# Kernel optimization log

Hardware: AMD Instinct MI355X
Metric: run time of the kernel (lower is better)

The kernel has to match this reference:

```python
import jax, jax.numpy as jnp
import numpy as np

D_IN = 1024
D_OUT = 1024


def setup_inputs() -> dict:
    key = jax.random.key(0)
    kx, kq, kk, kv = jax.random.split(key, 4)
    B, T = 8, 2048
    x = jax.random.normal(kx, (B, T, D_IN), dtype=jnp.float32)
    # torch Linear weight is (d_out, d_in); we store transposed (d_in, d_out)
    s = 1.0 / np.sqrt(D_IN)
    Wq = jax.random.uniform(kq, (D_IN, D_OUT), jnp.float32, -s, s)
    Wk = jax.random.uniform(kk, (D_IN, D_OUT), jnp.float32, -s, s)
    Wv = jax.random.uniform(kv, (D_IN, D_OUT), jnp.float32, -s, s)
    return {"x": x, "Wq": Wq, "Wk": Wk, "Wv": Wv}


def reference(x, Wq, Wk, Wv):
    # x: (B, T, d_in)
    T = x.shape[1]
    d_out = Wq.shape[1]
    q = jnp.einsum('btd,de->bte', x, Wq)  # (B,T,d_out)
    k = jnp.einsum('btd,de->bte', x, Wk)
    v = jnp.einsum('btd,de->bte', x, Wv)
    scores = jnp.einsum('bqe,bke->bqk', q, k)  # (B,T,T)
    causal = jnp.tril(jnp.ones((T, T), dtype=bool))  # True = keep
    scores = jnp.where(causal[None], scores, -jnp.inf)
    weights = jax.nn.softmax(scores / jnp.sqrt(jnp.asarray(d_out, x.dtype)), axis=-1)
    # dropout p=0.0 -> identity
    return jnp.einsum('bqk,bke->bqe', weights, v)  # (B,T,d_out)
```

## Files before the change

### kernel.cpp

```cpp
#include <hip/hip_runtime.h>

using u16 = unsigned short;
typedef __bf16 bf16x8 __attribute__((ext_vector_type(8)));
typedef unsigned short u16x8 __attribute__((ext_vector_type(8)));
typedef float floatx4 __attribute__((ext_vector_type(4)));

__device__ __forceinline__ u16 f2bf(float f) {
  union { float f; unsigned u; } c; c.f = f;
  unsigned u = c.u;
  u += 0x7fffu + ((u >> 16) & 1u);
  return (u16)(u >> 16);
}
__device__ __forceinline__ float bf2f(u16 h) {
  union { unsigned u; float f; } c; c.u = ((unsigned)h) << 16; return c.f;
}

__device__ __forceinline__ void st_out(float* p, float v) { *p = v; }
__device__ __forceinline__ void st_out(u16* p, float v) { *p = f2bf(v); }

__device__ __forceinline__ void load16(const u16* g, u16* l) {
  __builtin_amdgcn_global_load_lds(
      (const __attribute__((address_space(1))) void*)g,
      (__attribute__((address_space(3))) void*)l, 16, 0, 0);
}

#define TILE 128
#define BK 64

template<typename OutT>
__device__ __forceinline__ void gemm_core(
    const u16* __restrict__ A, int lda, long sA,
    const u16* __restrict__ Bt, int ldb, long sB,
    OutT* __restrict__ C, int ldc, long sC,
    int kmax, int bx, int by, int bz, int tid)
{
  __shared__ u16 As[TILE * BK];
  __shared__ u16 Bs[TILE * BK];

  const u16* Ab = A + bz * sA + (long)by * TILE * lda;
  const u16* Bb = Bt + bz * sB + (long)bx * TILE * ldb;

  int lane = tid & 63;
  int wm = ((tid >> 7) & 1) * 64;
  int wn = ((tid >> 6) & 1) * 64;

  floatx4 acc[4][4] = {};
  int arow = wm + (lane & 15);
  int brow = wn + (lane & 15);
  int q = lane >> 4;

  for (int k0 = 0; k0 < kmax; k0 += BK) {
    __syncthreads();
#pragma unroll
    for (int h = 0; h < 4; h++) {
      int cc = tid + h * 256;
      int row = cc >> 3, gm = (cc & 7) ^ (row & 7);
      load16(Ab + (long)row * lda + k0 + gm * 8, &As[cc * 8]);
    }
#pragma unroll
    for (int h = 0; h < 4; h++) {
      int cc = tid + h * 256;
      int row = cc >> 3, gm = (cc & 7) ^ (row & 7);
      load16(Bb + (long)row * ldb + k0 + gm * 8, &Bs[cc * 8]);
    }
    __builtin_amdgcn_s_waitcnt(0);
    __syncthreads();

#pragma unroll
    for (int kp = 0; kp < 2; kp++) {
      bf16x8 a[4], b[4];
#pragma unroll
      for (int i = 0; i < 4; i++) {
        int r = arow + i * 16;
        a[i] = *(const bf16x8*)&As[(r * 8 + ((kp * 4 + q) ^ (r & 7))) * 8];
      }
#pragma unroll
      for (int j = 0; j < 4; j++) {
        int r = brow + j * 16;
        b[j] = *(const bf16x8*)&Bs[(r * 8 + ((kp * 4 + q) ^ (r & 7))) * 8];
      }
#pragma unroll
      for (int i = 0; i < 4; i++)
#pragma unroll
        for (int j = 0; j < 4; j++)
          acc[i][j] = __builtin_amdgcn_mfma_f32_16x16x32_bf16(a[i], b[j], acc[i][j], 0, 0, 0);
    }
  }

  OutT* Cb = C + bz * sC;
  int colbase = bx * TILE + wn + (lane & 15);
  int rowbase = by * TILE + wm + ((lane >> 4) << 2);
#pragma unroll
  for (int i = 0; i < 4; i++)
#pragma unroll
    for (int j = 0; j < 4; j++) {
      int col = colbase + j * 16;
#pragma unroll
      for (int r = 0; r < 4; r++)
        st_out(&Cb[(long)(rowbase + i * 16 + r) * ldc + col], acc[i][j][r]);
    }
}

template<typename OutT>
__global__ __launch_bounds__(256, 2)
void gemm_rect(const u16* __restrict__ A, int lda, long sA,
               const u16* __restrict__ Bt, int ldb, long sB,
               OutT* __restrict__ C, int ldc, long sC, int K,
               int l2gx, int nO8s)
{
  int L = blockIdx.x;
  int t = ((L & 7) << nO8s) | (L >> 3);
  int bx = t & ((1 << l2gx) - 1), by = t >> l2gx;
  gemm_core<OutT>(A, lda, sA, Bt, ldb, sB, C, ldc, sC, K, bx, by, blockIdx.y, threadIdx.x);
}

__global__ __launch_bounds__(256, 2)
void gemm_proj(const u16* __restrict__ xb, const u16* __restrict__ NT,
               const u16* __restrict__ WvT, u16* __restrict__ Yb,
               u16* __restrict__ VT)
{
  int L = blockIdx.x;
  bool h = (L >= 1024);
  int LL = h ? L - 1024 : L;
  int t = ((LL & 7) << 7) | (LL >> 3);
  int bx = h ? (t & 127) : (t & 7);
  int by = h ? (t >> 7) : (t >> 3);
  gemm_core<u16>(h ? WvT : xb, 1024, 0L,
                 h ? xb : NT, 1024, 0L,
                 h ? VT : Yb, h ? 16384 : 1024, 0L,
                 1024, bx, by, 0, threadIdx.x);
}

__global__ __launch_bounds__(256, 2)
void gemm_tri(const u16* __restrict__ A, int lda, long sA,
              const u16* __restrict__ Bt, int ldb, long sB,
              u16* __restrict__ C, int ldc, long sC, int K)
{
  int tp = blockIdx.x;
  int t = (tp & 7) * 17 + (tp >> 3);
  int r = (int)((sqrtf(8.f * t + 1.f) - 1.f) * 0.5f);
  while ((r + 1) * (r + 2) / 2 <= t) ++r;
  while (r * (r + 1) / 2 > t) --r;
  int c = t - r * (r + 1) / 2;
  gemm_core<u16>(A, lda, sA, Bt, ldb, sB, C, ldc, sC, K, c, r, blockIdx.y, threadIdx.x);
}

__global__ __launch_bounds__(256, 2)
void gemm_opv(const u16* __restrict__ P, int lda, long sA,
              const u16* __restrict__ VT, int ldb, long sB,
              float* __restrict__ C, int ldc, long sC)
{
  int L = blockIdx.x;
  int j = L & 7, s = L >> 3;
  int by = (s < 8) ? 15 - j : j;
  int bx = s & 7;
  gemm_core<float>(P, lda, sA, VT, ldb, sB, C, ldc, sC,
                   (by + 1) * TILE, bx, by, blockIdx.y, threadIdx.x);
}

__global__ __launch_bounds__(256)
void cvt_x(const float4* __restrict__ x, u16* __restrict__ o, int n4, float scale)
{
  int i = blockIdx.x * 256 + threadIdx.x;
  if (i >= n4) return;
  float4 v = x[i];
  ushort4 r;
  r.x = f2bf(v.x * scale); r.y = f2bf(v.y * scale);
  r.z = f2bf(v.z * scale); r.w = f2bf(v.w * scale);
  *(ushort4*)(o + (long)i * 4) = r;
}

__global__ __launch_bounds__(256)
void cvt_w(const float* __restrict__ W, u16* __restrict__ O)
{
  const int D = 1024;
  __shared__ float t[64][65];
  int tid = threadIdx.x;
  int c = tid & 63, r = tid >> 6;
  int e0 = blockIdx.x * 64, d0 = blockIdx.y * 64;
  for (int rr = r; rr < 64; rr += 4)
    t[rr][c] = W[(long)(d0 + rr) * D + e0 + c];
  __syncthreads();
  for (int rr = r; rr < 64; rr += 4)
    O[(long)(e0 + rr) * D + d0 + c] = f2bf(t[c][rr]);
}

__global__ __launch_bounds__(256)
void softmax_bf16(u16* __restrict__ S)
{
  const int T = 2048;
  int row = blockIdx.x & (T - 1);
  u16* Prow = S + (long)blockIdx.x * T;
  int n = row + 1;
  int tid = threadIdx.x, lane = tid & 63, wid = tid >> 6;
  int i0 = tid * 8;

  u16x8 pv = *(const u16x8*)(Prow + i0);
  float v[8];
  float lmax = -3.0e38f;
#pragma unroll
  for (int j = 0; j < 8; j++) {
    v[j] = (i0 + j < n) ? bf2f(pv[j]) : -3.0e38f;
    lmax = fmaxf(lmax, v[j]);
  }
  __shared__ float red[8];
#pragma unroll
  for (int o = 32; o > 0; o >>= 1) lmax = fmaxf(lmax, __shfl_down(lmax, o, 64));
  if (lane == 0) red[wid] = lmax;
  __syncthreads();
  float m = fmaxf(fmaxf(red[0], red[1]), fmaxf(red[2], red[3]));

  float lsum = 0.f;
#pragma unroll
  for (int j = 0; j < 8; j++) {
    float e = (i0 + j < n) ? __expf(v[j] - m) : 0.f;
    v[j] = e;
    lsum += e;
  }
#pragma unroll
  for (int o = 32; o > 0; o >>= 1) lsum += __shfl_down(lsum, o, 64);
  if (lane == 0) red[4 + wid] = lsum;
  __syncthreads();
  float inv = 1.0f / (red[4] + red[5] + red[6] + red[7]);

  u16x8 w;
#pragma unroll
  for (int j = 0; j < 8; j++) w[j] = f2bf(v[j] * inv);
  *(u16x8*)(Prow + i0) = w;
}

extern "C" void kernel_launch(void* const* d_in, const int* in_sizes, int n_in,
                              void* d_out, int out_size, void* d_ws, size_t ws_size,
                              hipStream_t stream)
{
  const int B = 8, T = 2048, D = 1024;
  const float* x  = (const float*)d_in[0];
  const float* Wq = (const float*)d_in[1];
  const float* Wk = (const float*)d_in[2];
  const float* Wv = (const float*)d_in[3];
  float* out = (float*)d_out;
  char* ws = (char*)d_ws;

  u16* xb  = (u16*)(ws);
  u16* WvT = (u16*)(ws + (32ul << 20));
  u16* NT  = (u16*)(ws + (34ul << 20));
  u16* Yb  = (u16*)(ws + (36ul << 20));
  u16* Wqb = Yb;
  u16* Wkb = (u16*)(ws + (38ul << 20));
  u16* VT  = (u16*)(ws + (68ul << 20));
  u16* S   = (u16*)(ws + (100ul << 20));

  const size_t OFF_S = 100ul << 20;
  int NB = 8;
  while (NB > 1 && OFF_S + (size_t)NB * T * T * 2 > ws_size) NB >>= 1;

  cvt_x<<<(B * T * D / 4 + 255) / 256, 256, 0, stream>>>((const float4*)x, xb, B * T * D / 4, 1.0f);
  cvt_x<<<(D * D / 4 + 255) / 256, 256, 0, stream>>>((const float4*)Wq, Wqb, D * D / 4, 0.03125f);
  cvt_x<<<(D * D / 4 + 255) / 256, 256, 0, stream>>>((const float4*)Wk, Wkb, D * D / 4, 1.0f);
  cvt_w<<<dim3(16, 16), 256, 0, stream>>>(Wv, WvT);

  gemm_rect<u16><<<dim3(64, 1), 256, 0, stream>>>(
      Wkb, D, 0L, Wqb, D, 0L, NT, D, 0L, D, 3, 3);
  gemm_proj<<<dim3(2048, 1), 256, 0, stream>>>(xb, NT, WvT, Yb, VT);

  for (int b0 = 0; b0 < B; b0 += NB) {
    gemm_tri<<<dim3(136, NB), 256, 0, stream>>>(
        Yb + (long)b0 * T * D, D, (long)T * D,
        xb + (long)b0 * T * D, D, (long)T * D,
        S, T, (long)T * T, D);
    softmax_bf16<<<NB * T, 256, 0, stream>>>(S);
    gemm_opv<<<dim3(128, NB), 256, 0, stream>>>(
        S, T, (long)T * T,
        VT + (long)b0 * T, B * T, (long)T,
        out + (long)b0 * T * D, D, (long)T * D);
  }
}
```

Before: 370.2 us.

## Fuse attention pipeline into one cooperative persistent kernel with grid syncs

Measured after the change: 745.1 us. +101.3%, slower.

```diff
diff --git a/kernel.cpp b/kernel.cpp
--- a/kernel.cpp
+++ b/kernel.cpp
@@ -1,9 +1,15 @@
 #include <hip/hip_runtime.h>
+#include <hip/hip_cooperative_groups.h>
+
+namespace cg = cooperative_groups;
 
 using u16 = unsigned short;
 typedef __bf16 bf16x8 __attribute__((ext_vector_type(8)));
 typedef unsigned short u16x8 __attribute__((ext_vector_type(8)));
 typedef float floatx4 __attribute__((ext_vector_type(4)));
+
+#define D_ 1024
+#define T_ 2048
 
 __device__ __forceinline__ u16 f2bf(float f) {
   union { float f; unsigned u; } c; c.f = f;
@@ -29,17 +35,16 @@
 
 template<typename OutT>
 __device__ __forceinline__ void gemm_core(
-    const u16* __restrict__ A, int lda, long sA,
-    const u16* __restrict__ Bt, int ldb, long sB,
-    OutT* __restrict__ C, int ldc, long sC,
-    int kmax, int bx, int by, int bz, int tid)
-{
-  __shared__ u16 As[TILE * BK];
-  __shared__ u16 Bs[TILE * BK];
-
-  const u16* Ab = A + bz * sA + (long)by * TILE * lda;
-  const u16* Bb = Bt + bz * sB + (long)bx * TILE * ldb;
-
+    u16* As, u16* Bs,
+    const u16* __restrict__ A, int lda,
+    const u16* __restrict__ Bt, int ldb,
+    OutT* __restrict__ C, int ldc,
+    int kmax, int bx, int by)
+{
+  const u16* Ab = A + (long)by * TILE * lda;
+  const u16* Bb = Bt + (long)bx * TILE * ldb;
+
+  int tid = threadIdx.x;
   int lane = tid & 63;
   int wm = ((tid >> 7) & 1) * 64;
   int wn = ((tid >> 6) & 1) * 64;
@@ -87,7 +92,6 @@
     }
   }
 
-  OutT* Cb = C + bz * sC;
   int colbase = bx * TILE + wn + (lane & 15);
   int rowbase = by * TILE + wm + ((lane >> 4) << 2);
 #pragma unroll
@@ -97,143 +101,232 @@
       int col = colbase + j * 16;
 #pragma unroll
       for (int r = 0; r < 4; r++)
-        st_out(&Cb[(long)(rowbase + i * 16 + r) * ldc + col], acc[i][j][r]);
-    }
-}
-
-template<typename OutT>
+        st_out(&C[(long)(rowbase + i * 16 + r) * ldc + col], acc[i][j][r]);
+    }
+}
+
+
+__device__ __forceinline__ void ph_cvt(
+    const float* x, const float* Wq, const float* Wk, const float* Wv,
+    u16* xb, u16* Wqb, u16* Wkb, u16* WvT, char* smem, int b, int G)
+{
+  int tid = threadIdx.x;
+  for (int jb = b; jb < 9472; jb += G) {
+    if (jb < 9216) {
+      const float* src; u16* dst; float sc; long base;
+      if (jb < 8192)      { src = x;  dst = xb;  sc = 1.0f;     base = (long)jb * 2048; }
+      else if (jb < 8704) { src = Wq; dst = Wqb; sc = 0.03125f; base = (long)(jb - 8192) * 2048; }
+      else                { src = Wk; dst = Wkb; sc = 1.0f;     base = (long)(jb - 8704) * 2048; }
+      const float4* s4 = (const float4*)(src + base);
+      float4 v0 = s4[tid * 2], v1 = s4[tid * 2 + 1];
+      u16x8 r;
+      r[0] = f2bf(v0.x * sc); r[1] = f2bf(v0.y * sc);
+      r[2] = f2bf(v0.z * sc); r[3] = f2bf(v0.w * sc);
+      r[4] = f2bf(v1.x * sc); r[5] = f2bf(v1.y * sc);
+      r[6] = f2bf(v1.z * sc); r[7] = f2bf(v1.w * sc);
+      *(u16x8*)(dst + base + (long)tid * 8) = r;
+    } else {
+      int tj = jb - 9216;
+      int e0 = (tj & 15) * 64, d0 = (tj >> 4) * 64;
+      float* t = (float*)smem;
+      int c = tid & 63, r = tid >> 6;
+      __syncthreads();
+      for (int rr = r; rr < 64; rr += 4)
+        t[rr * 65 + c] = Wv[(long)(d0 + rr) * D_ + e0 + c];
+      __syncthreads();
+      for (int rr = r; rr < 64; rr += 4)
+        WvT[(long)(e0 + rr) * D_ + d0 + c] = f2bf(t[c * 65 + rr]);
+    }
+  }
+}
+
+__device__ __forceinline__ void ph_nt(const u16* Wqb, const u16* Wkb,
+                                      float* NTpart, u16* As, u16* Bs, int b, int G)
+{
+  for (int j = b; j < 256; j += G) {
+    int ks = j & 3, t = j >> 2;
+    gemm_core<float>(As, Bs, Wkb + ks * 256, D_, Wqb + ks * 256, D_,
+                     NTpart + (long)ks * D_ * D_, D_, 256, t & 7, t >> 3);
+  }
+}
+
+__device__ __forceinline__ void ph_ntred(const float* NTpart, u16* NT, int b, int G)
+{
+  for (int u = b * 256 + threadIdx.x; u < 131072; u += G * 256) {
+    long i = (long)u * 8;
+    float s[8];
+#pragma unroll
+    for (int k = 0; k < 8; k++) s[k] = 0.f;
+#pragma unroll
+    for (int p = 0; p < 4; p++) {
+      const float4* q4 = (const float4*)(NTpart + (long)p * D_ * D_ + i);
+      float4 a0 = q4[0], a1 = q4[1];
+      s[0] += a0.x; s[1] += a0.y; s[2] += a0.z; s[3] += a0.w;
+      s[4] += a1.x; s[5] += a1.y; s[6] += a1.z; s[7] += a1.w;
+    }
+    u16x8 o;
+#pragma unroll
+    for (int k = 0; k < 8; k++) o[k] = f2bf(s[k]);
+    *(u16x8*)(NT + i) = o;
+  }
+}
+
+__device__ __forceinline__ void ph_y(const u16* xb, const u16* NT, u16* Yb,
+                                     u16* As, u16* Bs, int b, int G)
+{
+  for (int j = b; j < 1024; j += G) {
+    int t = ((j & 7) << 7) | (j >> 3);
+    gemm_core<u16>(As, Bs, xb, D_, NT, D_, Yb, D_, D_, t & 7, t >> 3);
+  }
+}
+
+__device__ __forceinline__ void ph_trivt(const u16* Yb, const u16* xb, u16* S,
+                                         const u16* WvT, u16* VT,
+                                         u16* As, u16* Bs, int b, int G)
+{
+  for (int j = b; j < 2112; j += G) {
+    if (j < 1088) {
+      int zi = j / 136, tp = j - zi * 136;
+      int t = (tp & 7) * 17 + (tp >> 3);
+      int r = (int)((sqrtf(8.f * t + 1.f) - 1.f) * 0.5f);
+      while ((r + 1) * (r + 2) / 2 <= t) ++r;
+      while (r * (r + 1) / 2 > t) --r;
+      int c = t - r * (r + 1) / 2;
+      gemm_core<u16>(As, Bs, Yb + (long)zi * T_ * D_, D_,
+                     xb + (long)zi * T_ * D_, D_,
+                     S + (long)zi * T_ * T_, T_, D_, c, r);
+    } else {
+      int LL = j - 1088;
+      int xj = LL & 7, m = LL >> 3;
+      gemm_core<u16>(As, Bs, WvT, D_, xb, D_, VT, 8 * T_, D_,
+                     16 * xj + (m >> 3), m & 7);
+    }
+  }
+}
+
+__device__ __forceinline__ void ph_smx(u16* S, float* red, int b, int G)
+{
+  int tid = threadIdx.x, lane = tid & 63, wid = tid >> 6, i0 = tid * 8;
+  for (int rr = b; rr < 16384; rr += G) {
+    u16* Prow = S + (long)rr * T_;
+    int row = rr & (T_ - 1), n = row + 1, nw = ((row >> 7) + 1) << 7;
+    bool act = i0 < nw;
+    u16x8 pv = {};
+    if (act) pv = *(const u16x8*)(Prow + i0);
+    float v[8], lmax = -3.0e38f;
+#pragma unroll
+    for (int j = 0; j < 8; j++) {
+      v[j] = (i0 + j < n) ? bf2f(pv[j]) : -3.0e38f;
+      lmax = fmaxf(lmax, v[j]);
+    }
+#pragma unroll
+    for (int o = 32; o > 0; o >>= 1) lmax = fmaxf(lmax, __shfl_down(lmax, o, 64));
+    if (lane == 0) red[wid] = lmax;
+    __syncthreads();
+    float m = fmaxf(fmaxf(red[0], red[1]), fmaxf(red[2], red[3]));
+    float lsum = 0.f;
+#pragma unroll
+    for (int j = 0; j < 8; j++) {
+      float e = (i0 + j < n) ? __expf(v[j] - m) : 0.f;
+      v[j] = e;
+      lsum += e;
+    }
+#pragma unroll
+    for (int o = 32; o > 0; o >>= 1) lsum += __shfl_down(lsum, o, 64);
+    if (lane == 0) red[4 + wid] = lsum;
+    __syncthreads();
+    float inv = 1.0f / (red[4] + red[5] + red[6] + red[7]);
+    if (act) {
+      u16x8 w;
+#pragma unroll
+      for (int j = 0; j < 8; j++) w[j] = f2bf(v[j] * inv);
+      *(u16x8*)(Prow + i0) = w;
+    }
+    __syncthreads();
+  }
+}
+
+__device__ __forceinline__ void ph_opv(const u16* S, const u16* VT, float* out,
+                                       u16* As, u16* Bs, int b, int G)
+{
+  for (int J = b; J < 1024; J += G) {
+    int xj = J & 7, bt = (J >> 3) & 7, bx = (J >> 6) & 7, u = J >> 9;
+    int by = u ? xj : 15 - xj;
+    gemm_core<float>(As, Bs, S + (long)bt * T_ * T_, T_,
+                     VT + (long)bt * T_, 8 * T_,
+                     out + (long)bt * T_ * D_, D_, (by + 1) * TILE, bx, by);
+  }
+}
+
 __global__ __launch_bounds__(256, 2)
-void gemm_rect(const u16* __restrict__ A, int lda, long sA,
-               const u16* __restrict__ Bt, int ldb, long sB,
-               OutT* __restrict__ C, int ldc, long sC, int K,
-               int l2gx, int nO8s)
-{
-  int L = blockIdx.x;
-  int t = ((L & 7) << nO8s) | (L >> 3);
-  int bx = t & ((1 << l2gx) - 1), by = t >> l2gx;
-  gemm_core<OutT>(A, lda, sA, Bt, ldb, sB, C, ldc, sC, K, bx, by, blockIdx.y, threadIdx.x);
-}
-
-__global__ __launch_bounds__(256, 2)
-void gemm_proj(const u16* __restrict__ xb, const u16* __restrict__ NT,
-               const u16* __restrict__ WvT, u16* __restrict__ Yb,
-               u16* __restrict__ VT)
-{
-  int L = blockIdx.x;
-  bool h = (L >= 1024);
-  int LL = h ? L - 1024 : L;
-  int t = ((LL & 7) << 7) | (LL >> 3);
-  int bx = h ? (t & 127) : (t & 7);
-  int by = h ? (t >> 7) : (t >> 3);
-  gemm_core<u16>(h ? WvT : xb, 1024, 0L,
-                 h ? xb : NT, 1024, 0L,
-                 h ? VT : Yb, h ? 16384 : 1024, 0L,
-                 1024, bx, by, 0, threadIdx.x);
-}
-
-__global__ __launch_bounds__(256, 2)
-void gemm_tri(const u16* __restrict__ A, int lda, long sA,
-              const u16* __restrict__ Bt, int ldb, long sB,
-              u16* __restrict__ C, int ldc, long sC, int K)
-{
-  int tp = blockIdx.x;
-  int t = (tp & 7) * 17 + (tp >> 3);
-  int r = (int)((sqrtf(8.f * t + 1.f) - 1.f) * 0.5f);
-  while ((r + 1) * (r + 2) / 2 <= t) ++r;
-  while (r * (r + 1) / 2 > t) --r;
-  int c = t - r * (r + 1) / 2;
-  gemm_core<u16>(A, lda, sA, Bt, ldb, sB, C, ldc, sC, K, c, r, blockIdx.y, threadIdx.x);
-}
-
-__global__ __launch_bounds__(256, 2)
-void gemm_opv(const u16* __restrict__ P, int lda, long sA,
-              const u16* __restrict__ VT, int ldb, long sB,
-              float* __restrict__ C, int ldc, long sC)
-{
-  int L = blockIdx.x;
-  int j = L & 7, s = L >> 3;
-  int by = (s < 8) ? 15 - j : j;
-  int bx = s & 7;
-  gemm_core<float>(P, lda, sA, VT, ldb, sB, C, ldc, sC,
-                   (by + 1) * TILE, bx, by, blockIdx.y, threadIdx.x);
-}
-
-__global__ __launch_bounds__(256)
-void cvt_x(const float4* __restrict__ x, u16* __restrict__ o, int n4, float scale)
-{
-  int i = blockIdx.x * 256 + threadIdx.x;
-  if (i >= n4) return;
-  float4 v = x[i];
-  ushort4 r;
-  r.x = f2bf(v.x * scale); r.y = f2bf(v.y * scale);
-  r.z = f2bf(v.z * scale); r.w = f2bf(v.w * scale);
-  *(ushort4*)(o + (long)i * 4) = r;
-}
-
-__global__ __launch_bounds__(256)
-void cvt_w(const float* __restrict__ W, u16* __restrict__ O)
-{
-  const int D = 1024;
-  __shared__ float t[64][65];
-  int tid = threadIdx.x;
-  int c = tid & 63, r = tid >> 6;
-  int e0 = blockIdx.x * 64, d0 = blockIdx.y * 64;
-  for (int rr = r; rr < 64; rr += 4)
-    t[rr][c] = W[(long)(d0 + rr) * D + e0 + c];
-  __syncthreads();
-  for (int rr = r; rr < 64; rr += 4)
-    O[(long)(e0 + rr) * D + d0 + c] = f2bf(t[c][rr]);
-}
-
-__global__ __launch_bounds__(256)
-void softmax_bf16(u16* __restrict__ S)
-{
-  const int T = 2048;
-  int row = blockIdx.x & (T - 1);
-  u16* Prow = S + (long)blockIdx.x * T;
-  int n = row + 1;
-  int tid = threadIdx.x, lane = tid & 63, wid = tid >> 6;
-  int i0 = tid * 8;
-
-  u16x8 pv = *(const u16x8*)(Prow + i0);
-  float v[8];
-  float lmax = -3.0e38f;
-#pragma unroll
-  for (int j = 0; j < 8; j++) {
-    v[j] = (i0 + j < n) ? bf2f(pv[j]) : -3.0e38f;
-    lmax = fmaxf(lmax, v[j]);
-  }
+void attn_mega(const float* __restrict__ x, const float* __restrict__ Wq,
+               const float* __restrict__ Wk, const float* __restrict__ Wv,
+               u16* xb, u16* Wqb, u16* Wkb, u16* WvT,
+               float* NTpart, u16* NT, u16* Yb, u16* VT, u16* S, float* out)
+{
+  __shared__ __align__(16) char smem[32768];
+  u16* As = (u16*)smem;
+  u16* Bs = (u16*)(smem + 16384);
+  cg::grid_group grid = cg::this_grid();
+  int b = blockIdx.x, G = gridDim.x;
+
+  ph_cvt(x, Wq, Wk, Wv, xb, Wqb, Wkb, WvT, smem, b, G);
+  grid.sync();
+  ph_nt(Wqb, Wkb, NTpart, As, Bs, b, G);
+  grid.sync();
+  ph_ntred(NTpart, NT, b, G);
+  grid.sync();
+  ph_y(xb, NT, Yb, As, Bs, b, G);
+  grid.sync();
+  ph_trivt(Yb, xb, S, WvT, VT, As, Bs, b, G);
+  grid.sync();
+  ph_smx(S, (float*)smem, b, G);
+  grid.sync();
+  ph_opv(S, VT, out, As, Bs, b, G);
+}
+
+__global__ __launch_bounds__(256) void k_cvt(
+    const float* x, const float* Wq, const float* Wk, const float* Wv,
+    u16* xb, u16* Wqb, u16* Wkb, u16* WvT)
+{
+  __shared__ __align__(16) char smem[32768];
+  ph_cvt(x, Wq, Wk, Wv, xb, Wqb, Wkb, WvT, smem, blockIdx.x, gridDim.x);
+}
+__global__ __launch_bounds__(256, 2) void k_nt(const u16* Wqb, const u16* Wkb, float* NTpart)
+{
+  __shared__ __align__(16) char smem[32768];
+  ph_nt(Wqb, Wkb, NTpart, (u16*)smem, (u16*)(smem + 16384), blockIdx.x, gridDim.x);
+}
+__global__ __launch_bounds__(256) void k_ntred(const float* NTpart, u16* NT)
+{
+  ph_ntred(NTpart, NT, blockIdx.x, gridDim.x);
+}
+__global__ __launch_bounds__(256, 2) void k_y(const u16* xb, const u16* NT, u16* Yb)
+{
+  __shared__ __align__(16) char smem[32768];
+  ph_y(xb, NT, Yb, (u16*)smem, (u16*)(smem + 16384), blockIdx.x, gridDim.x);
+}
+__global__ __launch_bounds__(256, 2) void k_trivt(const u16* Yb, const u16* xb, u16* S,
+                                                  const u16* WvT, u16* VT)
+{
+  __shared__ __align__(16) char smem[32768];
+  ph_trivt(Yb, xb, S, WvT, VT, (u16*)smem, (u16*)(smem + 16384), blockIdx.x, gridDim.x);
+}
+__global__ __launch_bounds__(256) void k_smx(u16* S)
+{
   __shared__ float red[8];
-#pragma unroll
-  for (int o = 32; o > 0; o >>= 1) lmax = fmaxf(lmax, __shfl_down(lmax, o, 64));
-  if (lane == 0) red[wid] = lmax;
-  __syncthreads();
-  float m = fmaxf(fmaxf(red[0], red[1]), fmaxf(red[2], red[3]));
-
-  float lsum = 0.f;
-#pragma unroll
-  for (int j = 0; j < 8; j++) {
-    float e = (i0 + j < n) ? __expf(v[j] - m) : 0.f;
-    v[j] = e;
-    lsum += e;
-  }
-#pragma unroll
-  for (int o = 32; o > 0; o >>= 1) lsum += __shfl_down(lsum, o, 64);
-  if (lane == 0) red[4 + wid] = lsum;
-  __syncthreads();
-  float inv = 1.0f / (red[4] + red[5] + red[6] + red[7]);
-
-  u16x8 w;
-#pragma unroll
-  for (int j = 0; j < 8; j++) w[j] = f2bf(v[j] * inv);
-  *(u16x8*)(Prow + i0) = w;
+  ph_smx(S, red, blockIdx.x, gridDim.x);
+}
+__global__ __launch_bounds__(256, 2) void k_opv(const u16* S, const u16* VT, float* out)
+{
+  __shared__ __align__(16) char smem[32768];
+  ph_opv(S, VT, out, (u16*)smem, (u16*)(smem + 16384), blockIdx.x, gridDim.x);
 }
 
 extern "C" void kernel_launch(void* const* d_in, const int* in_sizes, int n_in,
                               void* d_out, int out_size, void* d_ws, size_t ws_size,
                               hipStream_t stream)
 {
-  const int B = 8, T = 2048, D = 1024;
   const float* x  = (const float*)d_in[0];
   const float* Wq = (const float*)d_in[1];
   const float* Wk = (const float*)d_in[2];
@@ -241,37 +334,33 @@
   float* out = (float*)d_out;
   char* ws = (char*)d_ws;
 
-  u16* xb  = (u16*)(ws);
-  u16* WvT = (u16*)(ws + (32ul << 20));
-  u16* NT  = (u16*)(ws + (34ul << 20));
-  u16* Yb  = (u16*)(ws + (36ul << 20));
-  u16* Wqb = Yb;
-  u16* Wkb = (u16*)(ws + (38ul << 20));
-  u16* VT  = (u16*)(ws + (68ul << 20));
-  u16* S   = (u16*)(ws + (100ul << 20));
-
-  const size_t OFF_S = 100ul << 20;
-  int NB = 8;
-  while (NB > 1 && OFF_S + (size_t)NB * T * T * 2 > ws_size) NB >>= 1;
-
-  cvt_x<<<(B * T * D / 4 + 255) / 256, 256, 0, stream>>>((const float4*)x, xb, B * T * D / 4, 1.0f);
-  cvt_x<<<(D * D / 4 + 255) / 256, 256, 0, stream>>>((const float4*)Wq, Wqb, D * D / 4, 0.03125f);
-  cvt_x<<<(D * D / 4 + 255) / 256, 256, 0, stream>>>((const float4*)Wk, Wkb, D * D / 4, 1.0f);
-  cvt_w<<<dim3(16, 16), 256, 0, stream>>>(Wv, WvT);
-
-  gemm_rect<u16><<<dim3(64, 1), 256, 0, stream>>>(
-      Wkb, D, 0L, Wqb, D, 0L, NT, D, 0L, D, 3, 3);
-  gemm_proj<<<dim3(2048, 1), 256, 0, stream>>>(xb, NT, WvT, Yb, VT);
-
-  for (int b0 = 0; b0 < B; b0 += NB) {
-    gemm_tri<<<dim3(136, NB), 256, 0, stream>>>(
-        Yb + (long)b0 * T * D, D, (long)T * D,
-        xb + (long)b0 * T * D, D, (long)T * D,
-        S, T, (long)T * T, D);
-    softmax_bf16<<<NB * T, 256, 0, stream>>>(S);
-    gemm_opv<<<dim3(128, NB), 256, 0, stream>>>(
-        S, T, (long)T * T,
-        VT + (long)b0 * T, B * T, (long)T,
-        out + (long)b0 * T * D, D, (long)T * D);
-  }
-}
+  u16*   xb     = (u16*)(ws);
+  u16*   WvT    = (u16*)(ws + (32ul  << 20));
+  u16*   NT     = (u16*)(ws + (34ul  << 20));
+  u16*   Yb     = (u16*)(ws + (36ul  << 20));
+  u16*   VT     = (u16*)(ws + (68ul  << 20));
+  u16*   S      = (u16*)(ws + (100ul << 20));
+  float* NTpart = (float*)(ws + (164ul << 20));
+  u16*   Wqb    = (u16*)(ws + (180ul << 20));
+  u16*   Wkb    = (u16*)(ws + (182ul << 20));
+
+  void* args[] = { &x, &Wq, &Wk, &Wv, &xb, &Wqb, &Wkb, &WvT,
+                   &NTpart, &NT, &Yb, &VT, &S, &out };
+  hipError_t e = hipLaunchCooperativeKernel((void*)attn_mega, dim3(512), dim3(256),
+                                            args, 0, stream);
+  if (e != hipSuccess) {
+    (void)hipGetLastError();
+    e = hipLaunchCooperativeKernel((void*)attn_mega, dim3(256), dim3(256),
+                                   args, 0, stream);
+  }
+  if (e != hipSuccess) {
+    (void)hipGetLastError();
+    k_cvt  <<<dim3(2368), 256, 0, stream>>>(x, Wq, Wk, Wv, xb, Wqb, Wkb, WvT);
+    k_nt   <<<dim3(256),  256, 0, stream>>>(Wqb, Wkb, NTpart);
+    k_ntred<<<dim3(512),  256, 0, stream>>>(NTpart, NT);
+    k_y    <<<dim3(1024), 256, 0, stream>>>(xb, NT, Yb);
+    k_trivt<<<dim3(2112), 256, 0, stream>>>(Yb, xb, S, WvT, VT);
+    k_smx  <<<dim3(4096), 256, 0, stream>>>(S);
+    k_opv  <<<dim3(1024), 256, 0, stream>>>(S, VT, out);
+  }
+}
```
